# Kernel tuning notes

Measured on AMD Instinct MI355X. Metric: run time of the kernel, lower is better.

Reference implementation:

```python
import jax, jax.numpy as jnp
import numpy as np

TEMPERATURE = 0.1
BATCH_SIZE = 64
EPS = 1e-8  # torch.nn.CosineSimilarity eps
NEG_INF = -1e30

B, C, D = 64, 16, 512  # batch, children per sample, feature dim


def setup_inputs() -> dict:
    key = jax.random.key(0)
    k1, k2, k3, k4 = jax.random.split(key, 4)
    children_is = jax.random.normal(k1, (B, C, D), dtype=jnp.float32)
    children_js = jax.random.normal(k2, (B, C, D), dtype=jnp.float32)
    partnet_ids = jnp.arange(B, dtype=jnp.int64 if jax.config.jax_enable_x64 else jnp.int32)
    neg_idx_j = jax.random.randint(k3, (B, B, C), 0, C)  # negatives drawn from children_js
    neg_idx_k = jax.random.randint(k4, (B, B, C), 0, C)  # negatives drawn from children_is
    return {
        "children_is": children_is,
        "children_js": children_js,
        "partnet_ids": partnet_ids,
        "neg_idx_j": neg_idx_j,
        "neg_idx_k": neg_idx_k,
    }


def _safe_norm(x, axis=-1):
    return jnp.maximum(jnp.sqrt(jnp.sum(x * x, axis=axis)), EPS)


def _ntxent(ci, cj, pids, nj, nk):
    b = ci.shape[0]
    fi = ci.reshape(b, -1)  # [B, L] flattened anchors
    fj = cj.reshape(b, -1)  # [B, L] flattened positives
    norm_i = _safe_norm(fi)

    # positive: cos(flat(children_i), flat(children_j[i])) / T
    pos = jnp.sum(fi * fj, axis=-1) / (norm_i * _safe_norm(fj))  # [B]

    src = jnp.arange(b)[None, :, None]  # broadcast source-sample index
    # gathered negatives: g*[i, j] = children_*[j, neg_idx[i, j]] flattened -> [B, B, L]
    gj = cj[src, nj].reshape(b, b, -1)
    gk = ci[src, nk].reshape(b, b, -1)

    sim_j = jnp.einsum('il,ijl->ij', fi, gj) / (norm_i[:, None] * _safe_norm(gj))
    sim_k = jnp.einsum('il,ijl->ij', fi, gk) / (norm_i[:, None] * _safe_norm(gk))

    # negative pair valid iff j != i and partnet ids differ
    eye = jnp.arange(b)
    mask = (eye[None, :] != eye[:, None]) & (pids[None, :] != pids[:, None])  # [B, B]

    logits = jnp.concatenate(
        [pos[:, None],
         jnp.where(mask, sim_j, NEG_INF),
         jnp.where(mask, sim_k, NEG_INF)], axis=1) / TEMPERATURE  # [B, 1+2B]

    # CrossEntropy with label 0, reduction='sum' over the batch of anchors
    loss = jnp.sum(-logits[:, 0] + jax.scipy.special.logsumexp(logits, axis=1))
    return loss / (2.0 * BATCH_SIZE)


def reference(children_is, children_js, partnet_ids, neg_idx_j, neg_idx_k):
    return _ntxent(children_is, children_js, partnet_ids, neg_idx_j, neg_idx_k)
```

## Files before the change

kernel.cpp:

```cpp
#include <hip/hip_runtime.h>
#include <math.h>

#define BB 64
#define CC 16
#define DD 512
#define LL 8192
#define EPSV 1e-8f
#define INVT 10.0f
#define NEGINF_T (-1e31f)

#define WS_N2I 0
#define WS_N2J 1024
#define WS_DJ  2048
#define WS_DK  6144
#define WS_POS 10240

__device__ __forceinline__ float dot4(float4 a, float4 b) {
    return a.x * b.x + a.y * b.y + a.z * b.z + a.w * b.w;
}

__device__ __forceinline__ float wave_reduce(float v) {
    #pragma unroll
    for (int off = 32; off; off >>= 1) v += __shfl_down(v, off);
    return v;
}

__global__ __launch_bounds__(256) void ntx_prep(const float* __restrict__ ci,
                                                const float* __restrict__ cj,
                                                float* __restrict__ ws,
                                                float* __restrict__ out) {
    const int b = blockIdx.x, tid = threadIdx.x;
    __shared__ float red[4];
    if (b < 512) {
        const int row  = b * 4 + (tid >> 6);
        const int lane = tid & 63;
        const int r    = row & 1023;
        const float4* src = (const float4*)(row < 1024 ? ci : cj);
        float4 v1 = src[r * 128 + lane];
        float4 v2 = src[r * 128 + 64 + lane];
        float acc = dot4(v1, v1) + dot4(v2, v2);
        acc = wave_reduce(acc);
        if (lane == 0) ws[(row < 1024 ? WS_N2I : WS_N2J) + r] = acc;
    } else {
        const int i = b - 512;
        if (b == 512 && tid == 0) out[0] = 0.f;
        const float4* fi = (const float4*)(ci + i * LL);
        const float4* fj = (const float4*)(cj + i * LL);
        float acc = 0.f;
        #pragma unroll
        for (int it = 0; it < 8; ++it) acc += dot4(fi[tid + 256 * it], fj[tid + 256 * it]);
        acc = wave_reduce(acc);
        if ((tid & 63) == 0) red[tid >> 6] = acc;
        __syncthreads();
        if (tid == 0) ws[WS_POS + i] = red[0] + red[1] + red[2] + red[3];
    }
}

__global__ __launch_bounds__(256) void ntx_sim(const float* __restrict__ ci,
                                               const float* __restrict__ cj,
                                               const int* __restrict__ nj,
                                               const int* __restrict__ nk,
                                               float* __restrict__ ws) {
    const int jt  = blockIdx.x;
    const int i   = blockIdx.y;
    const int tid = threadIdx.x;

    __shared__ int   sidx[2][4][16];
    __shared__ float red[4][2][4];

    if (tid < 64)        ((int*)sidx)[tid] = nj[i * 1024 + jt * 64 + tid];
    else if (tid < 128)  ((int*)sidx)[tid] = nk[i * 1024 + jt * 64 + (tid - 64)];

    const float4* fi4 = (const float4*)(ci + i * LL);
    float4 fiv[8];
    #pragma unroll
    for (int it = 0; it < 8; ++it) fiv[it] = fi4[tid + 256 * it];

    __syncthreads();

    const int d4   = tid & 127;
    const int half = tid >> 7;
    const float4* cj4 = (const float4*)cj;
    const float4* ci4 = (const float4*)ci;

    #pragma unroll
    for (int jj = 0; jj < 4; ++jj) {
        const int j = jt * 4 + jj;
        const float4* bj = cj4 + j * CC * 128;
        const float4* bk = ci4 + j * CC * 128;
        float aj = 0.f, ak = 0.f;
        #pragma unroll
        for (int it = 0; it < 8; ++it) {
            const int c = half + 2 * it;
            float4 vj = bj[sidx[0][jj][c] * 128 + d4];
            float4 vk = bk[sidx[1][jj][c] * 128 + d4];
            aj += dot4(fiv[it], vj);
            ak += dot4(fiv[it], vk);
        }
        aj = wave_reduce(aj);
        ak = wave_reduce(ak);
        if ((tid & 63) == 0) { red[jj][0][tid >> 6] = aj; red[jj][1][tid >> 6] = ak; }
    }
    __syncthreads();
    if (tid < 8) {
        const int jj = tid >> 1, side = tid & 1;
        float s = red[jj][side][0] + red[jj][side][1] + red[jj][side][2] + red[jj][side][3];
        ws[(side ? WS_DK : WS_DJ) + i * BB + jt * 4 + jj] = s;
    }
}

__global__ __launch_bounds__(64) void ntx_final(const int* __restrict__ pids,
                                                const int* __restrict__ nj,
                                                const int* __restrict__ nk,
                                                const float* __restrict__ ws,
                                                float* __restrict__ out) {
    const int i = blockIdx.x, j = threadIdx.x;
    __shared__ float sn2i[1024], sn2j[1024];
    const float4* n2i4 = (const float4*)(ws + WS_N2I);
    const float4* n2j4 = (const float4*)(ws + WS_N2J);
    #pragma unroll
    for (int t = 0; t < 4; ++t) {
        ((float4*)sn2i)[j + 64 * t] = n2i4[j + 64 * t];
        ((float4*)sn2j)[j + 64 * t] = n2j4[j + 64 * t];
    }
    __syncthreads();

    float si = 0.f, sjf = 0.f;
    #pragma unroll
    for (int c = 0; c < CC; ++c) { si += sn2i[i * CC + c]; sjf += sn2j[i * CC + c]; }
    const float ni = fmaxf(sqrtf(si), EPSV);
    const float l0 = ws[WS_POS + i] / (ni * fmaxf(sqrtf(sjf), EPSV)) * INVT;

    float gj = 0.f, gk = 0.f;
    #pragma unroll
    for (int c = 0; c < CC; ++c) {
        gj += sn2j[j * CC + nj[(i * BB + j) * CC + c]];
        gk += sn2i[j * CC + nk[(i * BB + j) * CC + c]];
    }

    const bool valid = (j != i) && (pids[j] != pids[i]);
    float lj = NEGINF_T, lk = NEGINF_T;
    if (valid) {
        const float inv = INVT / ni;
        lj = ws[WS_DJ + i * BB + j] / fmaxf(sqrtf(gj), EPSV) * inv;
        lk = ws[WS_DK + i * BB + j] / fmaxf(sqrtf(gk), EPSV) * inv;
    }

    float m = fmaxf(lj, lk);
    #pragma unroll
    for (int off = 32; off; off >>= 1) m = fmaxf(m, __shfl_xor(m, off));
    m = fmaxf(m, l0);

    float s = __expf(lj - m) + __expf(lk - m);
    s = wave_reduce(s);
    if (j == 0) {
        s += __expf(l0 - m);
        const float loss_i = -l0 + m + __logf(s);
        atomicAdd(out, loss_i * (1.0f / (2.0f * BB)));
    }
}

extern "C" void kernel_launch(void* const* d_in, const int* in_sizes, int n_in,
                              void* d_out, int out_size, void* d_ws, size_t ws_size,
                              hipStream_t stream) {
    const float* ci  = (const float*)d_in[0];
    const float* cj  = (const float*)d_in[1];
    const int*  pids = (const int*) d_in[2];
    const int*  nj   = (const int*) d_in[3];
    const int*  nk   = (const int*) d_in[4];
    float* ws  = (float*)d_ws;
    float* out = (float*)d_out;

    ntx_prep<<<576, 256, 0, stream>>>(ci, cj, ws, out);
    ntx_sim<<<dim3(16, BB), 256, 0, stream>>>(ci, cj, nj, nk, ws);
    ntx_final<<<BB, 64, 0, stream>>>(pids, nj, nk, ws, out);
}
```

Baseline: 80.09 us.

## Merge prep and similarity kernels into one launch; vectorize index loads

Folds the norm/positive-dot prep kernel and the gathered-negative similarity kernel into a single kernel with 1600 blocks, dispatching roles by block index. Since neither depends on the other's output, this removes one launch and the gap between them, letting both kinds of work run concurrently. The final kernel also loads negative indices as int4 instead of scalar ints. Shared memory usage per block becomes the union of the branches' arrays, which may slightly affect occupancy.

```diff
diff --git a/kernel.cpp b/kernel.cpp
--- a/kernel.cpp
+++ b/kernel.cpp
@@ -25,14 +25,61 @@
     return v;
 }
 
-__global__ __launch_bounds__(256) void ntx_prep(const float* __restrict__ ci,
+__global__ __launch_bounds__(256) void ntx_main(const float* __restrict__ ci,
                                                 const float* __restrict__ cj,
+                                                const int* __restrict__ nj,
+                                                const int* __restrict__ nk,
                                                 float* __restrict__ ws,
                                                 float* __restrict__ out) {
     const int b = blockIdx.x, tid = threadIdx.x;
-    __shared__ float red[4];
-    if (b < 512) {
-        const int row  = b * 4 + (tid >> 6);
+
+    if (b < 1024) {
+        __shared__ int   sidx[2][4][16];
+        __shared__ float red[4][2][4];
+        const int jt = b & 15;
+        const int i  = b >> 4;
+
+        if (tid < 64)        ((int*)sidx)[tid] = nj[i * 1024 + jt * 64 + tid];
+        else if (tid < 128)  ((int*)sidx)[tid] = nk[i * 1024 + jt * 64 + (tid - 64)];
+
+        const float4* fi4 = (const float4*)(ci + i * LL);
+        float4 fiv[8];
+        #pragma unroll
+        for (int it = 0; it < 8; ++it) fiv[it] = fi4[tid + 256 * it];
+
+        __syncthreads();
+
+        const int d4   = tid & 127;
+        const int half = tid >> 7;
+        const float4* cj4 = (const float4*)cj;
+        const float4* ci4 = (const float4*)ci;
+
+        #pragma unroll
+        for (int jj = 0; jj < 4; ++jj) {
+            const int j = jt * 4 + jj;
+            const float4* bj = cj4 + j * CC * 128;
+            const float4* bk = ci4 + j * CC * 128;
+            float aj = 0.f, ak = 0.f;
+            #pragma unroll
+            for (int it = 0; it < 8; ++it) {
+                const int c = half + 2 * it;
+                float4 vj = bj[sidx[0][jj][c] * 128 + d4];
+                float4 vk = bk[sidx[1][jj][c] * 128 + d4];
+                aj += dot4(fiv[it], vj);
+                ak += dot4(fiv[it], vk);
+            }
+            aj = wave_reduce(aj);
+            ak = wave_reduce(ak);
+            if ((tid & 63) == 0) { red[jj][0][tid >> 6] = aj; red[jj][1][tid >> 6] = ak; }
+        }
+        __syncthreads();
+        if (tid < 8) {
+            const int jj = tid >> 1, side = tid & 1;
+            float s = red[jj][side][0] + red[jj][side][1] + red[jj][side][2] + red[jj][side][3];
+            ws[(side ? WS_DK : WS_DJ) + i * BB + jt * 4 + jj] = s;
+        }
+    } else if (b < 1536) {
+        const int row  = (b - 1024) * 4 + (tid >> 6);
         const int lane = tid & 63;
         const int r    = row & 1023;
         const float4* src = (const float4*)(row < 1024 ? ci : cj);
@@ -42,70 +89,18 @@
         acc = wave_reduce(acc);
         if (lane == 0) ws[(row < 1024 ? WS_N2I : WS_N2J) + r] = acc;
     } else {
-        const int i = b - 512;
-        if (b == 512 && tid == 0) out[0] = 0.f;
+        __shared__ float red2[4];
+        const int i = b - 1536;
+        if (b == 1536 && tid == 0) out[0] = 0.f;
         const float4* fi = (const float4*)(ci + i * LL);
         const float4* fj = (const float4*)(cj + i * LL);
         float acc = 0.f;
         #pragma unroll
         for (int it = 0; it < 8; ++it) acc += dot4(fi[tid + 256 * it], fj[tid + 256 * it]);
         acc = wave_reduce(acc);
-        if ((tid & 63) == 0) red[tid >> 6] = acc;
+        if ((tid & 63) == 0) red2[tid >> 6] = acc;
         __syncthreads();
-        if (tid == 0) ws[WS_POS + i] = red[0] + red[1] + red[2] + red[3];
-    }
-}
-
-__global__ __launch_bounds__(256) void ntx_sim(const float* __restrict__ ci,
-                                               const float* __restrict__ cj,
-                                               const int* __restrict__ nj,
-                                               const int* __restrict__ nk,
-                                               float* __restrict__ ws) {
-    const int jt  = blockIdx.x;
-    const int i   = blockIdx.y;
-    const int tid = threadIdx.x;
-
-    __shared__ int   sidx[2][4][16];
-    __shared__ float red[4][2][4];
-
-    if (tid < 64)        ((int*)sidx)[tid] = nj[i * 1024 + jt * 64 + tid];
-    else if (tid < 128)  ((int*)sidx)[tid] = nk[i * 1024 + jt * 64 + (tid - 64)];
-
-    const float4* fi4 = (const float4*)(ci + i * LL);
-    float4 fiv[8];
-    #pragma unroll
-    for (int it = 0; it < 8; ++it) fiv[it] = fi4[tid + 256 * it];
-
-    __syncthreads();
-
-    const int d4   = tid & 127;
-    const int half = tid >> 7;
-    const float4* cj4 = (const float4*)cj;
-    const float4* ci4 = (const float4*)ci;
-
-    #pragma unroll
-    for (int jj = 0; jj < 4; ++jj) {
-        const int j = jt * 4 + jj;
-        const float4* bj = cj4 + j * CC * 128;
-        const float4* bk = ci4 + j * CC * 128;
-        float aj = 0.f, ak = 0.f;
-        #pragma unroll
-        for (int it = 0; it < 8; ++it) {
-            const int c = half + 2 * it;
-            float4 vj = bj[sidx[0][jj][c] * 128 + d4];
-            float4 vk = bk[sidx[1][jj][c] * 128 + d4];
-            aj += dot4(fiv[it], vj);
-            ak += dot4(fiv[it], vk);
-        }
-        aj = wave_reduce(aj);
-        ak = wave_reduce(ak);
-        if ((tid & 63) == 0) { red[jj][0][tid >> 6] = aj; red[jj][1][tid >> 6] = ak; }
-    }
-    __syncthreads();
-    if (tid < 8) {
-        const int jj = tid >> 1, side = tid & 1;
-        float s = red[jj][side][0] + red[jj][side][1] + red[jj][side][2] + red[jj][side][3];
-        ws[(side ? WS_DK : WS_DJ) + i * BB + jt * 4 + jj] = s;
+        if (tid == 0) ws[WS_POS + i] = red2[0] + red2[1] + red2[2] + red2[3];
     }
 }
 
@@ -131,11 +126,15 @@
     const float ni = fmaxf(sqrtf(si), EPSV);
     const float l0 = ws[WS_POS + i] / (ni * fmaxf(sqrtf(sjf), EPSV)) * INVT;
 
+    const int4* nj4 = (const int4*)(nj + (i * BB + j) * CC);
+    const int4* nk4 = (const int4*)(nk + (i * BB + j) * CC);
     float gj = 0.f, gk = 0.f;
     #pragma unroll
-    for (int c = 0; c < CC; ++c) {
-        gj += sn2j[j * CC + nj[(i * BB + j) * CC + c]];
-        gk += sn2i[j * CC + nk[(i * BB + j) * CC + c]];
+    for (int t = 0; t < 4; ++t) {
+        int4 a = nj4[t];
+        gj += sn2j[j * CC + a.x] + sn2j[j * CC + a.y] + sn2j[j * CC + a.z] + sn2j[j * CC + a.w];
+        int4 bq = nk4[t];
+        gk += sn2i[j * CC + bq.x] + sn2i[j * CC + bq.y] + sn2i[j * CC + bq.z] + sn2i[j * CC + bq.w];
     }
 
     const bool valid = (j != i) && (pids[j] != pids[i]);
@@ -171,7 +170,6 @@
     float* ws  = (float*)d_ws;
     float* out = (float*)d_out;
 
-    ntx_prep<<<576, 256, 0, stream>>>(ci, cj, ws, out);
-    ntx_sim<<<dim3(16, BB), 256, 0, stream>>>(ci, cj, nj, nk, ws);
+    ntx_main<<<1600, 256, 0, stream>>>(ci, cj, nj, nk, ws, out);
     ntx_final<<<BB, 64, 0, stream>>>(pids, nj, nk, ws, out);
 }
```

Result: faster. 77.61 us (-3.1%).
